# Performance work log

Hardware: AMD Instinct MI355X
Metric: run time of the kernel (lower is better)

The kernel has to match this reference:

```python
import jax, jax.numpy as jnp
import numpy as np

D_MODEL = 1024
NUM_HEADS = 16
HEAD_DIM = D_MODEL // NUM_HEADS
B, S = 2, 2048


def setup_inputs() -> dict:
    key = jax.random.key(0)
    ks = jax.random.split(key, 12)
    sc = 1.0 / np.sqrt(D_MODEL)
    return {
        "x": jax.random.normal(ks[0], (B, S, D_MODEL), dtype=jnp.float32),
        "Wq": jax.random.normal(ks[1], (D_MODEL, D_MODEL), dtype=jnp.float32) * sc,
        "bq": jnp.zeros((D_MODEL,), dtype=jnp.float32),
        "Wk": jax.random.normal(ks[2], (D_MODEL, D_MODEL), dtype=jnp.float32) * sc,
        "bk": jnp.zeros((D_MODEL,), dtype=jnp.float32),
        "Wv": jax.random.normal(ks[3], (D_MODEL, D_MODEL), dtype=jnp.float32) * sc,
        "bv": jnp.zeros((D_MODEL,), dtype=jnp.float32),
        "Wo": jax.random.normal(ks[4], (D_MODEL, D_MODEL), dtype=jnp.float32) * sc,
        "bo": jnp.zeros((D_MODEL,), dtype=jnp.float32),
        "gate": jax.random.normal(ks[5], (NUM_HEADS, HEAD_DIM), dtype=jnp.float32),
        "ent": jax.random.normal(ks[6], (NUM_HEADS, HEAD_DIM, HEAD_DIM), dtype=jnp.float32)
            * (1.0 / np.sqrt(HEAD_DIM)),
    }


def reference(x, Wq, bq, Wk, bk, Wv, bv, Wo, bo, gate, ent):
    b, s, _ = x.shape
    # QKV projections (torch Linear: x @ W^T + b)
    q = (x @ Wq.T + bq).reshape(b, s, NUM_HEADS, HEAD_DIM).transpose(0, 2, 1, 3)  # bhsd
    k = (x @ Wk.T + bk).reshape(b, s, NUM_HEADS, HEAD_DIM).transpose(0, 2, 1, 3)
    v = (x @ Wv.T + bv).reshape(b, s, NUM_HEADS, HEAD_DIM).transpose(0, 2, 1, 3)
    # superposition gate: per-head, per-dim sigmoid gate broadcast over sequence
    q = q * jax.nn.sigmoid(gate)[None, :, None, :]
    # entanglement: per-head small matmul on keys
    k = jnp.einsum("bhsd,hde->bhse", k, ent)
    scores = jnp.einsum("bhqd,bhkd->bhqk", q, k) / np.sqrt(HEAD_DIM)
    attn = jax.nn.softmax(scores, axis=-1)
    ctx = jnp.einsum("bhqk,bhkd->bhqd", attn, v)
    ctx = ctx.transpose(0, 2, 1, 3).reshape(b, s, D_MODEL)
    out = ctx @ Wo.T + bo
    return (out, attn)
```

## Files before the change

### kernel.cpp

```cpp
#include <hip/hip_runtime.h>
#include <hip/hip_bf16.h>

#define DM 1024
#define NH 16
#define HD 64
#define BATCH 2
#define SEQ 2048
#define MROWS (BATCH*SEQ)

typedef __attribute__((ext_vector_type(8))) short bf16x8;
typedef __attribute__((ext_vector_type(4))) short bf16x4;
typedef __attribute__((ext_vector_type(4))) float f32x4;
typedef __attribute__((ext_vector_type(4))) unsigned u32x4;

#define LOG2E 1.44269504088896f

__device__ __forceinline__ short f2b(float f) {
  union { float f; unsigned u; } x; x.f = f;
  unsigned r = x.u + 0x7fffu + ((x.u >> 16) & 1u);
  return (short)(r >> 16);
}

__device__ __forceinline__ unsigned cvtpk(float lo, float hi) {
  unsigned r;
  asm("v_cvt_pk_bf16_f32 %0, %1, %2" : "=v"(r) : "v"(lo), "v"(hi));
  return r;
}

__device__ __forceinline__ float nexp2(float x) {
  return __builtin_amdgcn_exp2f(x);
}

__device__ __forceinline__ void gload16(const void* g, void* l) {
  __builtin_amdgcn_global_load_lds((const __attribute__((address_space(1))) unsigned int*)g,
                                   (__attribute__((address_space(3))) unsigned int*)l, 16, 0, 0);
}


__global__ void k_conv(const float* __restrict__ src, short* __restrict__ dst, int n) {
  int i = (blockIdx.x * 256 + threadIdx.x) * 8;
  if (i >= n) return;
  const float4* s4 = (const float4*)(src + i);
  float4 a = s4[0], b = s4[1];
  bf16x8 o;
  o[0]=f2b(a.x); o[1]=f2b(a.y); o[2]=f2b(a.z); o[3]=f2b(a.w);
  o[4]=f2b(b.x); o[5]=f2b(b.y); o[6]=f2b(b.z); o[7]=f2b(b.w);
  *(bf16x8*)(dst + i) = o;
}

__global__ void k_conv_gate(const float* __restrict__ Wq, const float* __restrict__ gate,
                            short* __restrict__ dst) {
  int i = (blockIdx.x * 256 + threadIdx.x) * 8;
  int row = i >> 10;
  float sg = (0.125f * LOG2E) / (1.f + __expf(-gate[row]));
  const float4* s4 = (const float4*)(Wq + i);
  float4 a = s4[0], b = s4[1];
  bf16x8 o;
  o[0]=f2b(a.x*sg); o[1]=f2b(a.y*sg); o[2]=f2b(a.z*sg); o[3]=f2b(a.w*sg);
  o[4]=f2b(b.x*sg); o[5]=f2b(b.y*sg); o[6]=f2b(b.z*sg); o[7]=f2b(b.w*sg);
  *(bf16x8*)(dst + i) = o;
}

__global__ void k_went(const float* __restrict__ Wk, const float* __restrict__ ent,
                       short* __restrict__ dst) {
  int r = blockIdx.x;
  int h = r >> 6, e = r & 63;
  int c = blockIdx.y * 256 + threadIdx.x;
  float acc = 0.f;
#pragma unroll 8
  for (int d = 0; d < 64; ++d)
    acc += ent[h*4096 + d*64 + e] * Wk[(size_t)(h*64 + d)*DM + c];
  dst[(size_t)r*DM + c] = f2b(acc);
}

__global__ void k_bias(const float* __restrict__ bq, const float* __restrict__ bk,
                       const float* __restrict__ bv, const float* __restrict__ gate,
                       const float* __restrict__ ent, float* __restrict__ bcat) {
  int i = blockIdx.x * 256 + threadIdx.x;
  float v;
  if (i < 1024) {
    v = bq[i] * ((0.125f * LOG2E) / (1.f + __expf(-gate[i])));
  } else if (i < 2048) {
    int rr = i - 1024, h = rr >> 6, e = rr & 63;
    float a = 0.f;
    for (int d = 0; d < 64; ++d) a += bk[h*64 + d] * ent[h*4096 + d*64 + e];
    v = a;
  } else {
    v = bv[i - 2048];
  }
  bcat[i] = v;
}


template<int MODE>
__global__ __launch_bounds__(256) void gemm_bt(const short* __restrict__ A,
                                               const short* __restrict__ B,
                                               const float* __restrict__ bias,
                                               void* __restrict__ C,
                                               short* __restrict__ vt,
                                               int M, int N, int K) {
  __shared__ __align__(16) short As[128*64];
  __shared__ __align__(16) short Bs[128*64];
  const int t = threadIdx.x, l = t & 63, w = t >> 6;
  const int wr = w >> 1, wc = w & 1;
  const int bm = blockIdx.x, bn = blockIdx.y;
  const int row_l = l & 15, kg = l >> 4;
  f32x4 acc[4][4];
  {
    f32x4 z = {0.f, 0.f, 0.f, 0.f};
#pragma unroll
    for (int m = 0; m < 4; ++m)
#pragma unroll
      for (int n = 0; n < 4; ++n) acc[m][n] = z;
  }
  for (int k0 = 0; k0 < K; k0 += 64) {
#pragma unroll
    for (int i = 0; i < 4; ++i) {
      int idx = i * 256 + t;
      int row = idx >> 3, cb = (idx & 7) * 8;
      gload16(A + (size_t)(bm*128 + row)*K + k0 + cb, &As[idx*8]);
      gload16(B + (size_t)(bn*128 + row)*K + k0 + cb, &Bs[idx*8]);
    }
    __syncthreads();
#pragma unroll
    for (int ks = 0; ks < 2; ++ks) {
      bf16x8 af[4], bfv[4];
#pragma unroll
      for (int m = 0; m < 4; ++m)
        af[m] = *(const bf16x8*)&As[(wr*64 + m*16 + row_l)*64 + ks*32 + kg*8];
#pragma unroll
      for (int n = 0; n < 4; ++n)
        bfv[n] = *(const bf16x8*)&Bs[(wc*64 + n*16 + row_l)*64 + ks*32 + kg*8];
#pragma unroll
      for (int m = 0; m < 4; ++m)
#pragma unroll
        for (int n = 0; n < 4; ++n)
          acc[m][n] = __builtin_amdgcn_mfma_f32_16x16x32_bf16(af[m], bfv[n], acc[m][n], 0, 0, 0);
    }
    __syncthreads();
  }
  const int r0 = bm*128 + wr*64, c0 = bn*128 + wc*64;
  if (MODE == 1 && c0 >= 2048) {
    const int bb = (bm*128) >> 11;
#pragma unroll
    for (int n = 0; n < 4; ++n) {
      int cv = c0 + n*16 + row_l - 2048;
      int hh = cv >> 6, dd = cv & 63;
      float bvs = bias[c0 + n*16 + row_l];
      short* vrow = vt + ((size_t)((bb*16 + hh)*64 + dd))*SEQ;
#pragma unroll
      for (int m = 0; m < 4; ++m) {
        int s0 = (r0 + m*16 + kg*4) & (SEQ-1);
        bf16x4 o;
        o[0]=f2b(acc[m][n][0]+bvs); o[1]=f2b(acc[m][n][1]+bvs);
        o[2]=f2b(acc[m][n][2]+bvs); o[3]=f2b(acc[m][n][3]+bvs);
        *(bf16x4*)&vrow[s0] = o;
      }
    }
  } else {
#pragma unroll
    for (int n = 0; n < 4; ++n) {
      int col = c0 + n*16 + row_l;
      float bvs = bias[col];
#pragma unroll
      for (int m = 0; m < 4; ++m) {
#pragma unroll
        for (int r = 0; r < 4; ++r) {
          int row = r0 + m*16 + kg*4 + r;
          float v = acc[m][n][r] + bvs;
          if (MODE == 1) ((short*)C)[(size_t)row*2048 + col] = f2b(v);
          else           ((float*)C)[(size_t)row*N + col] = v;
        }
      }
    }
  }
}


__global__ __launch_bounds__(256) void attn_fused(const short* __restrict__ qk,
                                                  const short* __restrict__ vtg,
                                                  float* __restrict__ attn_out,
                                                  short* __restrict__ ctx) {
  __shared__ __align__(16) short Ks[2][64*64];
  __shared__ __align__(16) short Vt[2][64*64];
  const int t = threadIdx.x, l = t & 63, w = t >> 6;
  const int row_l = l & 15, kg = l >> 4;
  const int rsl = row_l & 7;
  const int blk = blockIdx.x;
  const int bh = blk >> 5, q0 = (blk & 31) * 64;
  const int b = bh >> 4, h = bh & 15;
  const short* Qp = qk + (size_t)b*SEQ*2048 + h*64;
  const short* Kp = qk + (size_t)b*SEQ*2048 + 1024 + h*64;
  const short* Vg = vtg + (size_t)bh*64*SEQ;
  float* attn_bh = attn_out + (size_t)bh*SEQ*SEQ;
  const int qw = q0 + w*16;

  const bf16x8 aq0 = *(const bf16x8*)(Qp + (size_t)(qw + row_l)*2048 + kg*8);
  const bf16x8 aq1 = *(const bf16x8*)(Qp + (size_t)(qw + row_l)*2048 + 32 + kg*8);

  const int a0 = t >> 3, a1 = a0 + 32;
  const int c8 = (t & 7) * 8;
  const int g0 = (a0 & 0x23) | ((a0 & 0x0C) << 1) | ((a0 & 0x10) >> 2);
  const int g1 = (a1 & 0x23) | ((a1 & 0x0C) << 1) | ((a1 & 0x10) >> 2);
  const int wof0 = a0*64 + (c8 ^ ((a0 & 7) << 3));
  const int wof1 = a1*64 + (c8 ^ ((a0 & 7) << 3));

  float rsum = 0.f;
  {
    bf16x8 rk0 = *(const bf16x8*)(Kp + (size_t)g0*2048 + c8);
    bf16x8 rk1 = *(const bf16x8*)(Kp + (size_t)g1*2048 + c8);
    *(bf16x8*)&Ks[0][wof0] = rk0;
    *(bf16x8*)&Ks[0][wof1] = rk1;
  }
  __syncthreads();
#pragma unroll 1
  for (int kt = 0; kt < 32; ++kt) {
    const int cur = kt & 1;
    bf16x8 rk0, rk1;
    if (kt < 31) {
      const short* kb = Kp + (size_t)(kt + 1)*64*2048;
      rk0 = *(const bf16x8*)(kb + (size_t)g0*2048 + c8);
      rk1 = *(const bf16x8*)(kb + (size_t)g1*2048 + c8);
    }
    __builtin_amdgcn_s_setprio(1);
#pragma unroll
    for (int nt = 0; nt < 4; ++nt) {
      const int row = nt*16 + row_l;
      bf16x8 k0 = *(const bf16x8*)&Ks[cur][row*64 + ((kg ^ rsl) << 3)];
      bf16x8 k1 = *(const bf16x8*)&Ks[cur][row*64 + (((kg|4) ^ rsl) << 3)];
      f32x4 s = {0.f, 0.f, 0.f, 0.f};
      s = __builtin_amdgcn_mfma_f32_16x16x32_bf16(k0, aq0, s, 0, 0, 0);
      s = __builtin_amdgcn_mfma_f32_16x16x32_bf16(k1, aq1, s, 0, 0, 0);
      rsum += (nexp2(s[0]) + nexp2(s[1])) + (nexp2(s[2]) + nexp2(s[3]));
    }
    __builtin_amdgcn_s_setprio(0);
    if (kt < 31) {
      *(bf16x8*)&Ks[cur^1][wof0] = rk0;
      *(bf16x8*)&Ks[cur^1][wof1] = rk1;
    }
    __syncthreads();
  }
  rsum += __shfl_xor(rsum, 16);
  rsum += __shfl_xor(rsum, 32);
  const float inv = 1.f / rsum;

  f32x4 actx[4];
  {
    f32x4 z = {0.f, 0.f, 0.f, 0.f};
#pragma unroll
    for (int e = 0; e < 4; ++e) actx[e] = z;
  }

  {
    bf16x8 rk0 = *(const bf16x8*)(Kp + (size_t)g0*2048 + c8);
    bf16x8 rk1 = *(const bf16x8*)(Kp + (size_t)g1*2048 + c8);
    bf16x8 rv0 = *(const bf16x8*)(Vg + (size_t)a0*SEQ + c8);
    bf16x8 rv1 = *(const bf16x8*)(Vg + (size_t)a1*SEQ + c8);
    *(bf16x8*)&Ks[0][wof0] = rk0;
    *(bf16x8*)&Ks[0][wof1] = rk1;
    *(bf16x8*)&Vt[0][wof0] = rv0;
    *(bf16x8*)&Vt[0][wof1] = rv1;
  }
  __syncthreads();
#pragma unroll 1
  for (int kt = 0; kt < 32; ++kt) {
    const int cur = kt & 1;
    bf16x8 rk0, rk1, rv0, rv1;
    if (kt < 31) {
      const short* kb = Kp + (size_t)(kt + 1)*64*2048;
      const short* vb = Vg + (kt + 1)*64;
      rk0 = *(const bf16x8*)(kb + (size_t)g0*2048 + c8);
      rk1 = *(const bf16x8*)(kb + (size_t)g1*2048 + c8);
      rv0 = *(const bf16x8*)(vb + (size_t)a0*SEQ + c8);
      rv1 = *(const bf16x8*)(vb + (size_t)a1*SEQ + c8);
    }
    f32x4 pf[4];
    __builtin_amdgcn_s_setprio(1);
#pragma unroll
    for (int nt = 0; nt < 4; ++nt) {
      const int row = nt*16 + row_l;
      bf16x8 k0 = *(const bf16x8*)&Ks[cur][row*64 + ((kg ^ rsl) << 3)];
      bf16x8 k1 = *(const bf16x8*)&Ks[cur][row*64 + (((kg|4) ^ rsl) << 3)];
      f32x4 s = {0.f, 0.f, 0.f, 0.f};
      s = __builtin_amdgcn_mfma_f32_16x16x32_bf16(k0, aq0, s, 0, 0, 0);
      s = __builtin_amdgcn_mfma_f32_16x16x32_bf16(k1, aq1, s, 0, 0, 0);
      f32x4 p;
      p[0] = nexp2(s[0]) * inv; p[1] = nexp2(s[1]) * inv;
      p[2] = nexp2(s[2]) * inv; p[3] = nexp2(s[3]) * inv;
      *(f32x4*)&attn_bh[(size_t)(qw + row_l)*SEQ + kt*64 + (nt&2)*16 + kg*8 + (nt&1)*4] = p;
      pf[nt] = p;
    }
#pragma unroll
    for (int hh = 0; hh < 2; ++hh) {
      u32x4 pq;
      pq[0] = cvtpk(pf[2*hh][0],   pf[2*hh][1]);
      pq[1] = cvtpk(pf[2*hh][2],   pf[2*hh][3]);
      pq[2] = cvtpk(pf[2*hh+1][0], pf[2*hh+1][1]);
      pq[3] = cvtpk(pf[2*hh+1][2], pf[2*hh+1][3]);
      bf16x8 pb = *(bf16x8*)&pq;
      const int vslot = ((kg | (hh << 2)) ^ rsl) << 3;
#pragma unroll
      for (int e = 0; e < 4; ++e) {
        bf16x8 va = *(const bf16x8*)&Vt[cur][(e*16 + row_l)*64 + vslot];
        actx[e] = __builtin_amdgcn_mfma_f32_16x16x32_bf16(va, pb, actx[e], 0, 0, 0);
      }
    }
    __builtin_amdgcn_s_setprio(0);
    if (kt < 31) {
      *(bf16x8*)&Ks[cur^1][wof0] = rk0;
      *(bf16x8*)&Ks[cur^1][wof1] = rk1;
      *(bf16x8*)&Vt[cur^1][wof0] = rv0;
      *(bf16x8*)&Vt[cur^1][wof1] = rv1;
    }
    __syncthreads();
  }
#pragma unroll
  for (int e = 0; e < 4; ++e) {
    int2 o;
    o.x = (int)cvtpk(actx[e][0], actx[e][1]);
    o.y = (int)cvtpk(actx[e][2], actx[e][3]);
    *(int2*)&ctx[(size_t)(b*SEQ + qw + row_l)*DM + h*64 + e*16 + kg*4] = o;
  }
}


extern "C" void kernel_launch(void* const* d_in, const int* in_sizes, int n_in,
                              void* d_out, int out_size, void* d_ws, size_t ws_size,
                              hipStream_t stream) {
  const float* x    = (const float*)d_in[0];
  const float* Wq   = (const float*)d_in[1];
  const float* bq   = (const float*)d_in[2];
  const float* Wk   = (const float*)d_in[3];
  const float* bk   = (const float*)d_in[4];
  const float* Wv   = (const float*)d_in[5];
  const float* bv   = (const float*)d_in[6];
  const float* Wo   = (const float*)d_in[7];
  const float* bo   = (const float*)d_in[8];
  const float* gate = (const float*)d_in[9];
  const float* ent  = (const float*)d_in[10];

  char* ws = (char*)d_ws;
  short* xb   = (short*)(ws);
  short* Wcat = (short*)(ws + ((size_t)8  << 20));
  short* Wob  = (short*)(ws + ((size_t)14 << 20));
  float* bcat = (float*)(ws + ((size_t)16 << 20));
  short* qkb  = (short*)(ws + ((size_t)17 << 20));
  short* vtg  = (short*)(ws + ((size_t)33 << 20));
  short* ctxb = xb;

  float* outp  = (float*)d_out;
  float* attnp = outp + (size_t)MROWS * DM;

  k_conv<<<2048, 256, 0, stream>>>(x, xb, MROWS*DM);
  k_conv_gate<<<512, 256, 0, stream>>>(Wq, gate, Wcat);
  k_went<<<dim3(1024, 4), 256, 0, stream>>>(Wk, ent, Wcat + (size_t)1024*DM);
  k_conv<<<512, 256, 0, stream>>>(Wv, Wcat + (size_t)2048*DM, 1024*1024);
  k_conv<<<512, 256, 0, stream>>>(Wo, Wob, 1024*1024);
  k_bias<<<12, 256, 0, stream>>>(bq, bk, bv, gate, ent, bcat);

  gemm_bt<1><<<dim3(32, 24), 256, 0, stream>>>(xb, Wcat, bcat, qkb, vtg, MROWS, 3072, DM);
  attn_fused<<<1024, 256, 0, stream>>>(qkb, vtg, attnp, ctxb);
  gemm_bt<0><<<dim3(32, 8), 256, 0, stream>>>(ctxb, Wob, bo, outp, nullptr, MROWS, DM, DM);
}
```

Before: 282.4 us.

## Add XCD-aware block remapping and smaller-tile output projection GEMM

Remaps GEMM workgroup indices so that tiles dispatched to the same XCD are contiguous, improving L2 reuse of the A and B panels. Replaces the output-projection GEMM with a 64x128-tile variant, doubling the block count to fill more CUs. The smaller tile lowers per-block reuse and the remap assumes round-robin dispatch across 8 XCDs.

Result: no change. 285.8 us (+1.2%).

```diff
diff --git a/kernel.cpp b/kernel.cpp
--- a/kernel.cpp
+++ b/kernel.cpp
@@ -92,7 +92,7 @@
 }
 
 
-template<int MODE>
+template<int MODE, int LGX>
 __global__ __launch_bounds__(256) void gemm_bt(const short* __restrict__ A,
                                                const short* __restrict__ B,
                                                const float* __restrict__ bias,
@@ -103,7 +103,10 @@
   __shared__ __align__(16) short Bs[128*64];
   const int t = threadIdx.x, l = t & 63, w = t >> 6;
   const int wr = w >> 1, wc = w & 1;
-  const int bm = blockIdx.x, bn = blockIdx.y;
+  const int lin = blockIdx.x + (blockIdx.y << LGX);
+  const int nwg = gridDim.x * gridDim.y;
+  const int virt = (lin & 7) * (nwg >> 3) + (lin >> 3);
+  const int bm = virt & ((1 << LGX) - 1), bn = virt >> LGX;
   const int row_l = l & 15, kg = l >> 4;
   f32x4 acc[4][4];
   {
@@ -171,6 +174,75 @@
           if (MODE == 1) ((short*)C)[(size_t)row*2048 + col] = f2b(v);
           else           ((float*)C)[(size_t)row*N + col] = v;
         }
+      }
+    }
+  }
+}
+
+__global__ __launch_bounds__(256) void gemm_bt_small(const short* __restrict__ A,
+                                                     const short* __restrict__ B,
+                                                     const float* __restrict__ bias,
+                                                     float* __restrict__ C,
+                                                     int M, int N, int K) {
+  __shared__ __align__(16) short As[64*64];
+  __shared__ __align__(16) short Bs[128*64];
+  const int t = threadIdx.x, l = t & 63, w = t >> 6;
+  const int wr = w >> 1, wc = w & 1;
+  const int lin = blockIdx.x + (blockIdx.y << 6);
+  const int nwg = gridDim.x * gridDim.y;
+  const int virt = (lin & 7) * (nwg >> 3) + (lin >> 3);
+  const int bm = virt & 63, bn = virt >> 6;
+  const int row_l = l & 15, kg = l >> 4;
+  f32x4 acc[2][4];
+  {
+    f32x4 z = {0.f, 0.f, 0.f, 0.f};
+#pragma unroll
+    for (int m = 0; m < 2; ++m)
+#pragma unroll
+      for (int n = 0; n < 4; ++n) acc[m][n] = z;
+  }
+  for (int k0 = 0; k0 < K; k0 += 64) {
+#pragma unroll
+    for (int i = 0; i < 2; ++i) {
+      int idx = i * 256 + t;
+      int row = idx >> 3, cb = (idx & 7) * 8;
+      gload16(A + (size_t)(bm*64 + row)*K + k0 + cb, &As[idx*8]);
+    }
+#pragma unroll
+    for (int i = 0; i < 4; ++i) {
+      int idx = i * 256 + t;
+      int row = idx >> 3, cb = (idx & 7) * 8;
+      gload16(B + (size_t)(bn*128 + row)*K + k0 + cb, &Bs[idx*8]);
+    }
+    __syncthreads();
+#pragma unroll
+    for (int ks = 0; ks < 2; ++ks) {
+      bf16x8 af[2], bfv[4];
+#pragma unroll
+      for (int m = 0; m < 2; ++m)
+        af[m] = *(const bf16x8*)&As[(wr*32 + m*16 + row_l)*64 + ks*32 + kg*8];
+#pragma unroll
+      for (int n = 0; n < 4; ++n)
+        bfv[n] = *(const bf16x8*)&Bs[(wc*64 + n*16 + row_l)*64 + ks*32 + kg*8];
+#pragma unroll
+      for (int m = 0; m < 2; ++m)
+#pragma unroll
+        for (int n = 0; n < 4; ++n)
+          acc[m][n] = __builtin_amdgcn_mfma_f32_16x16x32_bf16(af[m], bfv[n], acc[m][n], 0, 0, 0);
+    }
+    __syncthreads();
+  }
+  const int r0 = bm*64 + wr*32, c0 = bn*128 + wc*64;
+#pragma unroll
+  for (int n = 0; n < 4; ++n) {
+    int col = c0 + n*16 + row_l;
+    float bvs = bias[col];
+#pragma unroll
+    for (int m = 0; m < 2; ++m) {
+#pragma unroll
+      for (int r = 0; r < 4; ++r) {
+        int row = r0 + m*16 + kg*4 + r;
+        C[(size_t)row*N + col] = acc[m][n][r] + bvs;
       }
     }
   }
@@ -358,7 +430,7 @@
   k_conv<<<512, 256, 0, stream>>>(Wo, Wob, 1024*1024);
   k_bias<<<12, 256, 0, stream>>>(bq, bk, bv, gate, ent, bcat);
 
-  gemm_bt<1><<<dim3(32, 24), 256, 0, stream>>>(xb, Wcat, bcat, qkb, vtg, MROWS, 3072, DM);
+  gemm_bt<1, 5><<<dim3(32, 24), 256, 0, stream>>>(xb, Wcat, bcat, qkb, vtg, MROWS, 3072, DM);
   attn_fused<<<1024, 256, 0, stream>>>(qkb, vtg, attnp, ctxb);
-  gemm_bt<0><<<dim3(32, 8), 256, 0, stream>>>(ctxb, Wob, bo, outp, nullptr, MROWS, DM, DM);
-}
+  gemm_bt_small<<<dim3(64, 8), 256, 0, stream>>>(ctxb, Wob, bo, outp, MROWS, DM, DM);
+}
```
